# Performance work log

Measured on AMD Instinct MI355X. Metric: run time of the kernel, lower is better.

Reference implementation:

```python
import jax, jax.numpy as jnp
import numpy as np

BLOCK_SIZE = 128
FP8_MAX = 448.0
IN_FEATURES = 4096
OUT_FEATURES = 4096


def _fp8_round(x):
    # Simulate float8_e4m3fn storage; fall back to clamp-only if dtype unsupported.
    try:
        return x.astype(jnp.float8_e4m3fn).astype(jnp.float32)
    except Exception:
        return x


def setup_inputs() -> dict:
    key = jax.random.key(0)
    kx, kw = jax.random.split(key)
    x = jax.random.normal(kx, (2, 4096, IN_FEATURES), dtype=jnp.float32)
    # Kaiming-uniform-ish init, then block-quantize exactly as fp8_block_quantize does.
    bound = 1.0 / np.sqrt(IN_FEATURES)
    w = jax.random.uniform(kw, (OUT_FEATURES, IN_FEATURES), minval=-bound, maxval=bound, dtype=jnp.float32)
    w_blocks = w.reshape(-1, BLOCK_SIZE)  # (n_blocks, 128); 4096*4096 divisible by 128
    block_abs_max = jnp.maximum(jnp.max(jnp.abs(w_blocks), axis=-1), 1e-12)
    fp8_scales = block_abs_max / FP8_MAX  # (n_blocks,)
    w_scaled = jnp.clip(w_blocks / fp8_scales[:, None], -FP8_MAX, FP8_MAX)
    weight_q = _fp8_round(w_scaled).reshape(OUT_FEATURES, IN_FEATURES)
    bias = jnp.zeros((OUT_FEATURES,), dtype=jnp.float32)
    return {"x": x, "weight_q": weight_q, "fp8_scales": fp8_scales, "bias": bias}


def reference(x, weight_q, fp8_scales, bias):
    # Block-wise dequantize: flatten weight, scale each 128-element block.
    w_blocks = weight_q.reshape(-1, BLOCK_SIZE)            # (n_blocks, 128)
    w = (w_blocks * fp8_scales[:, None]).reshape(OUT_FEATURES, IN_FEATURES)
    # F.linear: y = x @ w.T + b
    return jnp.einsum('bsk,nk->bsn', x, w) + bias
```

## Files before the change

### kernel.cpp

```cpp
#include <hip/hip_runtime.h>


#define M_DIM 8192
#define N_DIM 4096
#define K_DIM 4096
#define K_TILES (K_DIM / 64)

typedef short s16x8 __attribute__((ext_vector_type(8)));
typedef float f32x4 __attribute__((ext_vector_type(4)));
typedef unsigned int u32x4 __attribute__((ext_vector_type(4)));

__device__ __forceinline__ unsigned int pack2_bf16(float a, float b) {
    unsigned int ua = __float_as_uint(a);
    unsigned int ub = __float_as_uint(b);
    unsigned int ra = ((ua + 0x7fffu + ((ua >> 16) & 1u)) >> 16) & 0xffffu;
    unsigned int rb = (ub + 0x7fffu + ((ub >> 16) & 1u)) & 0xffff0000u;
    return ra | rb;
}

__global__ __launch_bounds__(256) void cvt_fused_kernel(
    const float4* __restrict__ x, const float4* __restrict__ wq,
    const float* __restrict__ scales,
    u32x4* __restrict__ xo, u32x4* __restrict__ wo) {
    const int NX   = (M_DIM * K_DIM) / 8;
    const int NTOT = NX + (N_DIM * K_DIM) / 8;
    const int stride = gridDim.x * blockDim.x;
    for (int u = blockIdx.x * blockDim.x + threadIdx.x; u < NTOT; u += stride) {
        if (u < NX) {
            const float4 a = x[2 * u];
            const float4 b = x[2 * u + 1];
            u32x4 r;
            r[0] = pack2_bf16(a.x, a.y); r[1] = pack2_bf16(a.z, a.w);
            r[2] = pack2_bf16(b.x, b.y); r[3] = pack2_bf16(b.z, b.w);
            xo[u] = r;
        } else {
            const int v = u - NX;
            const float s = scales[v >> 4];
            float4 a = wq[2 * v];
            float4 b = wq[2 * v + 1];
            a.x *= s; a.y *= s; a.z *= s; a.w *= s;
            b.x *= s; b.y *= s; b.z *= s; b.w *= s;
            u32x4 r;
            r[0] = pack2_bf16(a.x, a.y); r[1] = pack2_bf16(a.z, a.w);
            r[2] = pack2_bf16(b.x, b.y); r[3] = pack2_bf16(b.z, b.w);
            wo[v] = r;
        }
    }
}

__device__ __forceinline__ void async_copy16(const void* g, void* l) {
    __builtin_amdgcn_global_load_lds(
        (const __attribute__((address_space(1))) unsigned int*)g,
        (__attribute__((address_space(3))) unsigned int*)l,
        16, 0, 0);
}


#define STAGE_A_HALF(h, ktt, bufb) do {                                        \
    const unsigned short* g_ = gA0 + (ktt) * 64 + (h) * (64 * K_DIM);          \
    async_copy16(g_,               ldsA + (bufb) + (h) * 8192 + aOff);         \
    async_copy16(g_ + 128 * K_DIM, ldsA + (bufb) + (h) * 8192 + 16384 + aOff); \
  } while (0)

#define STAGE_B_HALF(h, ktt, bufb) do {                                        \
    const unsigned short* g_ = gB0 + (ktt) * 64 + (h) * (32 * K_DIM);          \
    async_copy16(g_,               ldsB + (bufb) + (h) * 4096 + bOff);         \
    async_copy16(g_ + 128 * K_DIM, ldsB + (bufb) + (h) * 4096 + 16384 + bOff); \
  } while (0)

#define READ_AF(dst, qm, bufb) do {                                            \
    _Pragma("unroll")                                                          \
    for (int i_ = 0; i_ < 4; ++i_) {                                           \
      dst[i_][0] = *(const s16x8*)(ldsA + (bufb) + aRowB + ((qm)*64 + i_*16)*128 + kk0); \
      dst[i_][1] = *(const s16x8*)(ldsA + (bufb) + aRowB + ((qm)*64 + i_*16)*128 + kk1); \
    }                                                                          \
  } while (0)

#define READ_BF(dst, qn, bufb) do {                                            \
    _Pragma("unroll")                                                          \
    for (int j_ = 0; j_ < 2; ++j_) {                                           \
      dst[j_][0] = *(const s16x8*)(ldsB + (bufb) + bRowB + ((qn)*32 + j_*16)*128 + kk0); \
      dst[j_][1] = *(const s16x8*)(ldsB + (bufb) + bRowB + ((qn)*32 + j_*16)*128 + kk1); \
    }                                                                          \
  } while (0)

#define MFMA32(qm, AF, BX, BY) do {                                            \
    __builtin_amdgcn_s_setprio(1);                                             \
    _Pragma("unroll")                                                          \
    for (int i_ = 0; i_ < 4; ++i_) {                                           \
      _Pragma("unroll")                                                        \
      for (int j_ = 0; j_ < 2; ++j_) {                                         \
        acc[(qm)*4+i_][j_] = __builtin_amdgcn_mfma_f32_16x16x32_bf16(          \
            AF[i_][0], BX[j_][0], acc[(qm)*4+i_][j_], 0, 0, 0);                \
        acc[(qm)*4+i_][j_] = __builtin_amdgcn_mfma_f32_16x16x32_bf16(          \
            AF[i_][1], BX[j_][1], acc[(qm)*4+i_][j_], 0, 0, 0);                \
      }                                                                        \
      _Pragma("unroll")                                                        \
      for (int j_ = 0; j_ < 2; ++j_) {                                         \
        acc[(qm)*4+i_][2+j_] = __builtin_amdgcn_mfma_f32_16x16x32_bf16(        \
            AF[i_][0], BY[j_][0], acc[(qm)*4+i_][2+j_], 0, 0, 0);              \
        acc[(qm)*4+i_][2+j_] = __builtin_amdgcn_mfma_f32_16x16x32_bf16(        \
            AF[i_][1], BY[j_][1], acc[(qm)*4+i_][2+j_], 0, 0, 0);              \
      }                                                                        \
    }                                                                          \
    __builtin_amdgcn_s_setprio(0);                                             \
  } while (0)

__global__ __launch_bounds__(512, 2) void gemm_bt_kernel(
    const unsigned short* __restrict__ A,
    const unsigned short* __restrict__ B,
    const float* __restrict__ bias,
    float* __restrict__ C)
{
    __shared__ __align__(16) char lds[131072];
    char* ldsA = lds;
    char* ldsB = lds + 32768;

    const int t = threadIdx.x;
    const int l = t & 63;
    const int w = t >> 6;
    const int wr = w >> 2;
    const int wc = w & 3;

    int id = blockIdx.x;
    id = (id & 7) * 64 + (id >> 3);
    const int m0 = (id >> 4) * 256;
    const int n0 = (id & 15) * 256;

    const int trow = t >> 3;
    const int tcol = ((t & 7) * 8) ^ ((trow & 7) * 8);
    const unsigned short* gA0 = A + (long)(m0 + trow) * K_DIM + tcol;
    const int brow = ((t >> 8) * 64) + ((t & 255) >> 3);
    const unsigned short* gB0 = B + (long)(n0 + brow) * K_DIM + tcol;
    const int aOff = t * 16;
    const int bOff = ((t >> 8) * 8192) + ((t & 255) * 16);

    const int aRowB = (wr * 128 + (l & 15)) * 128;
    const int bRowB = (wc * 64  + (l & 15)) * 128;
    const int kx  = (l >> 4) * 16;
    const int sw  = (l & 7) * 16;
    const int kk0 = kx ^ sw;
    const int kk1 = (64 + kx) ^ sw;

    f32x4 acc[8][4] = {};
    s16x8 af[4][2], bfX[2][2], bfY[2][2];

    STAGE_A_HALF(0, 0, 0);
    STAGE_B_HALF(0, 0, 0);
    STAGE_B_HALF(1, 0, 0);
    STAGE_A_HALF(1, 0, 0);

    for (int kt = 0; kt < K_TILES - 1; ++kt) {
        const int cb = (kt & 1) * 65536;
        const int nb = 65536 - cb;
        STAGE_A_HALF(0, kt + 1, nb);
        STAGE_B_HALF(0, kt + 1, nb);
        asm volatile("s_waitcnt vmcnt(4)" ::: "memory");
        __builtin_amdgcn_s_barrier();
        __builtin_amdgcn_sched_barrier(0);
        READ_AF(af, 0, cb);
        READ_BF(bfX, 0, cb);
        READ_BF(bfY, 1, cb);
        MFMA32(0, af, bfX, bfY);
        STAGE_B_HALF(1, kt + 1, nb);
        STAGE_A_HALF(1, kt + 1, nb);
        __builtin_amdgcn_s_barrier();
        __builtin_amdgcn_sched_barrier(0);
        READ_AF(af, 1, cb);
        MFMA32(1, af, bfX, bfY);
    }
    {
        const int cb = ((K_TILES - 1) & 1) * 65536;
        asm volatile("s_waitcnt vmcnt(0)" ::: "memory");
        __builtin_amdgcn_s_barrier();
        __builtin_amdgcn_sched_barrier(0);
        READ_AF(af, 0, cb);
        READ_BF(bfX, 0, cb);
        READ_BF(bfY, 1, cb);
        MFMA32(0, af, bfX, bfY);
        __builtin_amdgcn_s_barrier();
        __builtin_amdgcn_sched_barrier(0);
        READ_AF(af, 1, cb);
        MFMA32(1, af, bfX, bfY);
    }

    const int q4 = (l >> 4) * 4;
#pragma unroll
    for (int nf = 0; nf < 4; ++nf) {
        const int col = n0 + wc * 64 + nf * 16 + (l & 15);
        const float bv = bias[col];
#pragma unroll
        for (int mf = 0; mf < 8; ++mf) {
            const long row = m0 + wr * 128 + mf * 16 + q4;
#pragma unroll
            for (int r = 0; r < 4; ++r) {
                C[(row + r) * N_DIM + col] = acc[mf][nf][r] + bv;
            }
        }
    }
}

extern "C" void kernel_launch(void* const* d_in, const int* in_sizes, int n_in,
                              void* d_out, int out_size, void* d_ws, size_t ws_size,
                              hipStream_t stream) {
    const float* x      = (const float*)d_in[0];
    const float* wq     = (const float*)d_in[1];
    const float* scales = (const float*)d_in[2];
    const float* bias   = (const float*)d_in[3];
    float* out = (float*)d_out;

    unsigned short* x_bf = (unsigned short*)d_ws;
    unsigned short* w_bf = x_bf + (size_t)M_DIM * K_DIM;

    cvt_fused_kernel<<<2048, 256, 0, stream>>>(
        (const float4*)x, (const float4*)wq, scales,
        (u32x4*)x_bf, (u32x4*)w_bf);

    gemm_bt_kernel<<<dim3(512), dim3(512), 0, stream>>>(x_bf, w_bf, bias, out);
}
```

Measured before the change: 497.7 us.

## Fuse fp32-to-bf16 conversion and weight dequantization into the GEMM main loop

```diff
diff --git a/kernel.cpp b/kernel.cpp
--- a/kernel.cpp
+++ b/kernel.cpp
@@ -18,54 +18,43 @@
     return ra | rb;
 }
 
-__global__ __launch_bounds__(256) void cvt_fused_kernel(
-    const float4* __restrict__ x, const float4* __restrict__ wq,
-    const float* __restrict__ scales,
-    u32x4* __restrict__ xo, u32x4* __restrict__ wo) {
-    const int NX   = (M_DIM * K_DIM) / 8;
-    const int NTOT = NX + (N_DIM * K_DIM) / 8;
-    const int stride = gridDim.x * blockDim.x;
-    for (int u = blockIdx.x * blockDim.x + threadIdx.x; u < NTOT; u += stride) {
-        if (u < NX) {
-            const float4 a = x[2 * u];
-            const float4 b = x[2 * u + 1];
-            u32x4 r;
-            r[0] = pack2_bf16(a.x, a.y); r[1] = pack2_bf16(a.z, a.w);
-            r[2] = pack2_bf16(b.x, b.y); r[3] = pack2_bf16(b.z, b.w);
-            xo[u] = r;
-        } else {
-            const int v = u - NX;
-            const float s = scales[v >> 4];
-            float4 a = wq[2 * v];
-            float4 b = wq[2 * v + 1];
-            a.x *= s; a.y *= s; a.z *= s; a.w *= s;
-            b.x *= s; b.y *= s; b.z *= s; b.w *= s;
-            u32x4 r;
-            r[0] = pack2_bf16(a.x, a.y); r[1] = pack2_bf16(a.z, a.w);
-            r[2] = pack2_bf16(b.x, b.y); r[3] = pack2_bf16(b.z, b.w);
-            wo[v] = r;
-        }
-    }
-}
-
-__device__ __forceinline__ void async_copy16(const void* g, void* l) {
-    __builtin_amdgcn_global_load_lds(
-        (const __attribute__((address_space(1))) unsigned int*)g,
-        (__attribute__((address_space(3))) unsigned int*)l,
-        16, 0, 0);
-}
-
-
-#define STAGE_A_HALF(h, ktt, bufb) do {                                        \
-    const unsigned short* g_ = gA0 + (ktt) * 64 + (h) * (64 * K_DIM);          \
-    async_copy16(g_,               ldsA + (bufb) + (h) * 8192 + aOff);         \
-    async_copy16(g_ + 128 * K_DIM, ldsA + (bufb) + (h) * 8192 + 16384 + aOff); \
-  } while (0)
-
-#define STAGE_B_HALF(h, ktt, bufb) do {                                        \
-    const unsigned short* g_ = gB0 + (ktt) * 64 + (h) * (32 * K_DIM);          \
-    async_copy16(g_,               ldsB + (bufb) + (h) * 4096 + bOff);         \
-    async_copy16(g_ + 128 * K_DIM, ldsB + (bufb) + (h) * 4096 + 16384 + bOff); \
+
+#define ISSUE_A(c) do {                                                        \
+    const float* p0_ = X + (long)(m0 + (2*(c))*64   + rT) * K_DIM + kcN;       \
+    const float* p1_ = X + (long)(m0 + (2*(c)+1)*64 + rT) * K_DIM + kcN;       \
+    ga0 = *(const float4*)p0_; ga1 = *(const float4*)(p0_ + 4);                \
+    ga2 = *(const float4*)p1_; ga3 = *(const float4*)(p1_ + 4);                \
+  } while (0)
+
+#define ISSUE_B(c) do {                                                        \
+    const float* q0_ = Wq + (long)(n0 + (2*(c))*64   + rT) * K_DIM + kcN;      \
+    const float* q1_ = Wq + (long)(n0 + (2*(c)+1)*64 + rT) * K_DIM + kcN;      \
+    gb0 = *(const float4*)q0_; gb1 = *(const float4*)(q0_ + 4);                \
+    gb2 = *(const float4*)q1_; gb3 = *(const float4*)(q1_ + 4);                \
+  } while (0)
+
+#define WRITE_A(c, nb) do {                                                    \
+    u32x4 r0_, r1_;                                                            \
+    r0_[0] = pack2_bf16(ga0.x, ga0.y); r0_[1] = pack2_bf16(ga0.z, ga0.w);      \
+    r0_[2] = pack2_bf16(ga1.x, ga1.y); r0_[3] = pack2_bf16(ga1.z, ga1.w);      \
+    r1_[0] = pack2_bf16(ga2.x, ga2.y); r1_[1] = pack2_bf16(ga2.z, ga2.w);      \
+    r1_[2] = pack2_bf16(ga3.x, ga3.y); r1_[3] = pack2_bf16(ga3.z, ga3.w);      \
+    *(u32x4*)(ldsA + (nb) + (2*(c))*8192   + wAddr) = r0_;                     \
+    *(u32x4*)(ldsA + (nb) + (2*(c)+1)*8192 + wAddr) = r1_;                     \
+  } while (0)
+
+#define WRITE_B(c, nb, sA, sB) do {                                            \
+    u32x4 r0_, r1_;                                                            \
+    r0_[0] = pack2_bf16(gb0.x*(sA), gb0.y*(sA));                               \
+    r0_[1] = pack2_bf16(gb0.z*(sA), gb0.w*(sA));                               \
+    r0_[2] = pack2_bf16(gb1.x*(sA), gb1.y*(sA));                               \
+    r0_[3] = pack2_bf16(gb1.z*(sA), gb1.w*(sA));                               \
+    r1_[0] = pack2_bf16(gb2.x*(sB), gb2.y*(sB));                               \
+    r1_[1] = pack2_bf16(gb2.z*(sB), gb2.w*(sB));                               \
+    r1_[2] = pack2_bf16(gb3.x*(sB), gb3.y*(sB));                               \
+    r1_[3] = pack2_bf16(gb3.z*(sB), gb3.w*(sB));                               \
+    *(u32x4*)(ldsB + (nb) + (2*(c))*8192   + wAddr) = r0_;                     \
+    *(u32x4*)(ldsB + (nb) + (2*(c)+1)*8192 + wAddr) = r1_;                     \
   } while (0)
 
 #define READ_AF(dst, qm, bufb) do {                                            \
@@ -106,9 +95,10 @@
     __builtin_amdgcn_s_setprio(0);                                             \
   } while (0)
 
-__global__ __launch_bounds__(512, 2) void gemm_bt_kernel(
-    const unsigned short* __restrict__ A,
-    const unsigned short* __restrict__ B,
+__global__ __launch_bounds__(512, 2) void gemm_fused_kernel(
+    const float* __restrict__ X,
+    const float* __restrict__ Wq,
+    const float* __restrict__ Sc,
     const float* __restrict__ bias,
     float* __restrict__ C)
 {
@@ -127,13 +117,12 @@
     const int m0 = (id >> 4) * 256;
     const int n0 = (id & 15) * 256;
 
-    const int trow = t >> 3;
-    const int tcol = ((t & 7) * 8) ^ ((trow & 7) * 8);
-    const unsigned short* gA0 = A + (long)(m0 + trow) * K_DIM + tcol;
-    const int brow = ((t >> 8) * 64) + ((t & 255) >> 3);
-    const unsigned short* gB0 = B + (long)(n0 + brow) * K_DIM + tcol;
-    const int aOff = t * 16;
-    const int bOff = ((t >> 8) * 8192) + ((t & 255) * 16);
+    const int rT = t >> 3;
+    const int wAddr = ((rT * 128 + (t & 7) * 16) ^ ((rT & 7) * 16));
+    const int sIdx0 = (n0 + 0 * 64 + rT) * 32;
+    const int sIdx1 = (n0 + 1 * 64 + rT) * 32;
+    const int sIdx2 = (n0 + 2 * 64 + rT) * 32;
+    const int sIdx3 = (n0 + 3 * 64 + rT) * 32;
 
     const int aRowB = (wr * 128 + (l & 15)) * 128;
     const int bRowB = (wc * 64  + (l & 15)) * 128;
@@ -144,34 +133,48 @@
 
     f32x4 acc[8][4] = {};
     s16x8 af[4][2], bfX[2][2], bfY[2][2];
-
-    STAGE_A_HALF(0, 0, 0);
-    STAGE_B_HALF(0, 0, 0);
-    STAGE_B_HALF(1, 0, 0);
-    STAGE_A_HALF(1, 0, 0);
+    float4 ga0, ga1, ga2, ga3, gb0, gb1, gb2, gb3;
+
+    {
+        const int kcN = (t & 7) * 8;
+        const float s0 = Sc[sIdx0], s1 = Sc[sIdx1];
+        const float s2 = Sc[sIdx2], s3 = Sc[sIdx3];
+        ISSUE_A(0); ISSUE_B(0);
+        WRITE_A(0, 0); WRITE_B(0, 0, s0, s1);
+        ISSUE_A(1); ISSUE_B(1);
+        WRITE_A(1, 0); WRITE_B(1, 0, s2, s3);
+        asm volatile("s_waitcnt lgkmcnt(0)" ::: "memory");
+    }
 
     for (int kt = 0; kt < K_TILES - 1; ++kt) {
         const int cb = (kt & 1) * 65536;
         const int nb = 65536 - cb;
-        STAGE_A_HALF(0, kt + 1, nb);
-        STAGE_B_HALF(0, kt + 1, nb);
-        asm volatile("s_waitcnt vmcnt(4)" ::: "memory");
+        const int kcN = (kt + 1) * 64 + (t & 7) * 8;
+        ISSUE_A(0);
+        ISSUE_B(0);
+        const int sblk = (kt + 1) >> 1;
+        const float s0 = Sc[sIdx0 + sblk], s1 = Sc[sIdx1 + sblk];
+        const float s2 = Sc[sIdx2 + sblk], s3 = Sc[sIdx3 + sblk];
         __builtin_amdgcn_s_barrier();
         __builtin_amdgcn_sched_barrier(0);
         READ_AF(af, 0, cb);
         READ_BF(bfX, 0, cb);
         READ_BF(bfY, 1, cb);
         MFMA32(0, af, bfX, bfY);
-        STAGE_B_HALF(1, kt + 1, nb);
-        STAGE_A_HALF(1, kt + 1, nb);
+        WRITE_A(0, nb);
+        ISSUE_A(1);
+        WRITE_B(0, nb, s0, s1);
+        ISSUE_B(1);
         __builtin_amdgcn_s_barrier();
         __builtin_amdgcn_sched_barrier(0);
         READ_AF(af, 1, cb);
         MFMA32(1, af, bfX, bfY);
+        WRITE_A(1, nb);
+        WRITE_B(1, nb, s2, s3);
+        asm volatile("s_waitcnt lgkmcnt(0)" ::: "memory");
     }
     {
         const int cb = ((K_TILES - 1) & 1) * 65536;
-        asm volatile("s_waitcnt vmcnt(0)" ::: "memory");
         __builtin_amdgcn_s_barrier();
         __builtin_amdgcn_sched_barrier(0);
         READ_AF(af, 0, cb);
@@ -209,12 +212,6 @@
     const float* bias   = (const float*)d_in[3];
     float* out = (float*)d_out;
 
-    unsigned short* x_bf = (unsigned short*)d_ws;
-    unsigned short* w_bf = x_bf + (size_t)M_DIM * K_DIM;
-
-    cvt_fused_kernel<<<2048, 256, 0, stream>>>(
-        (const float4*)x, (const float4*)wq, scales,
-        (u32x4*)x_bf, (u32x4*)w_bf);
-
-    gemm_bt_kernel<<<dim3(512), dim3(512), 0, stream>>>(x_bf, w_bf, bias, out);
+    gemm_fused_kernel<<<dim3(512), dim3(512), 0, stream>>>(
+        x, wq, scales, bias, out);
 }
```

New measurement: 629.7 us. +26.5%, slower.
